# Kernel tuning notes

Measured on AMD Instinct MI355X. Metric: run time of the kernel, lower is better.

## Reference

```python
import jax, jax.numpy as jnp
import numpy as np

B, S, D, H = 2, 2048, 1024, 16
DK = D // H
THETA = 10000.0


def _freqs_cos_sin(dim, seq_len, theta=THETA):
    # matches precompute_freqs_cis: freqs over full d_model, pairs of adjacent dims
    inv = 1.0 / theta ** (np.arange(0, dim, 2)[: dim // 2].astype(np.float32) / dim)
    t = np.arange(seq_len, dtype=np.float32)
    ang = np.outer(t, inv)  # [S, D/2]
    return jnp.asarray(np.cos(ang)), jnp.asarray(np.sin(ang))


def setup_inputs() -> dict:
    key = jax.random.key(0)
    ks = jax.random.split(key, 11)
    sc = 1.0 / np.sqrt(D)
    cos, sin = _freqs_cos_sin(D, S)
    return {
        "query": jax.random.normal(ks[0], (B, S, D), jnp.float32),
        "key": jax.random.normal(ks[1], (B, S, D), jnp.float32),
        "value": jax.random.normal(ks[2], (B, S, D), jnp.float32),
        "wq": jax.random.normal(ks[3], (D, D), jnp.float32) * sc,
        "bq": jnp.zeros((D,), jnp.float32),
        "wk": jax.random.normal(ks[4], (D, D), jnp.float32) * sc,
        "bk": jnp.zeros((D,), jnp.float32),
        "wv": jax.random.normal(ks[5], (D, D), jnp.float32) * sc,
        "bv": jnp.zeros((D,), jnp.float32),
        "wo": jax.random.normal(ks[6], (D, D), jnp.float32) * sc,
        "bo": jnp.zeros((D,), jnp.float32),
        "cos": cos,  # [S, D/2]
        "sin": sin,  # [S, D/2]
    }


def _rope(x, cos, sin):
    # x: [B,S,D]; pairs are adjacent elements along D (view_as_complex semantics)
    xr = x.reshape(*x.shape[:-1], -1, 2)  # [B,S,D/2,2]
    x0, x1 = xr[..., 0], xr[..., 1]
    c, s = cos[None], sin[None]  # broadcast over batch
    o0 = x0 * c - x1 * s
    o1 = x0 * s + x1 * c
    return jnp.stack([o0, o1], axis=-1).reshape(x.shape)


def reference(query, key, value, wq, bq, wk, bk, wv, bv, wo, bo, cos, sin):
    q = query @ wq.T + bq
    k = key @ wk.T + bk
    v = value @ wv.T + bv
    q = _rope(q, cos, sin)
    k = _rope(k, cos, sin)
    # split heads: [B,S,D] -> [B,H,S,DK]
    q = q.reshape(B, S, H, DK).transpose(0, 2, 1, 3)
    k = k.reshape(B, S, H, DK).transpose(0, 2, 1, 3)
    v = v.reshape(B, S, H, DK).transpose(0, 2, 1, 3)
    scores = jnp.einsum("bhqd,bhkd->bhqk", q, k) / jnp.sqrt(jnp.float32(DK))
    attn = jax.nn.softmax(scores, axis=-1)  # dropout is identity in eval
    out = jnp.einsum("bhqk,bhkd->bhqd", attn, v)
    out = out.transpose(0, 2, 1, 3).reshape(B, S, D)
    return out @ wo.T + bo
```

## Files before the change

kernel.cpp:

```cpp
#include <hip/hip_runtime.h>
#include <hip/hip_fp16.h>

typedef _Float16 f16;
using f16x8 = __attribute__((ext_vector_type(8))) _Float16;
using h2 = __attribute__((ext_vector_type(2))) __fp16;
using f32x4 = __attribute__((ext_vector_type(4))) float;
using f32x16 = __attribute__((ext_vector_type(16))) float;

#define LOG2E 1.4426950408889634f

__device__ __forceinline__ void gload16(const void* g, void* l) {
  __builtin_amdgcn_global_load_lds(
      (const __attribute__((address_space(1))) void*)g,
      (__attribute__((address_space(3))) void*)l, 16, 0, 0);
}

__device__ __forceinline__ float b32(h2 x) { return __builtin_bit_cast(float, x); }
__device__ __forceinline__ unsigned u32(h2 x) { return __builtin_bit_cast(unsigned, x); }

__global__ __launch_bounds__(256) void convert_k(
    const float* __restrict__ q, const float* __restrict__ k, const float* __restrict__ v,
    const float* __restrict__ wq, const float* __restrict__ wk,
    const float* __restrict__ wv, const float* __restrict__ wo,
    f16* __restrict__ dst) {
  const size_t SEG = (size_t)4 * 1024 * 1024;
  size_t i = ((size_t)blockIdx.x * 256 + threadIdx.x) * 8;
  const float* src; size_t off;
  if (i < SEG)            { src = q;  off = i; }
  else if (i < 2 * SEG)   { src = k;  off = i - SEG; }
  else if (i < 3 * SEG)   { src = v;  off = i - 2 * SEG; }
  else {
    size_t wi = i - 3 * SEG;
    int s = (int)(wi >> 20);
    src = (s == 0) ? wq : (s == 1) ? wk : (s == 2) ? wv : wo;
    off = wi & ((1u << 20) - 1);
  }
  float4 a = *(const float4*)(src + off);
  float4 b = *(const float4*)(src + off + 4);
  f16x8 o;
  o[0] = (f16)a.x; o[1] = (f16)a.y; o[2] = (f16)a.z; o[3] = (f16)a.w;
  o[4] = (f16)b.x; o[5] = (f16)b.y; o[6] = (f16)b.z; o[7] = (f16)b.w;
  *(f16x8*)(dst + i) = o;
}

template <int QKV>
__global__ __launch_bounds__(256) void gemm_k(
    const f16* __restrict__ Abase, const f16* __restrict__ Wbase,
    const float* __restrict__ b0, const float* __restrict__ b1, const float* __restrict__ b2,
    const float* __restrict__ cosT, const float* __restrict__ sinT,
    f16* __restrict__ qh, f16* __restrict__ kh, f16* __restrict__ vt,
    float* __restrict__ outF) {
  __shared__ f16 sm[6][128 * 32];
  int tid = threadIdx.x, wid = tid >> 6, lane = tid & 63;
  int z = QKV ? blockIdx.z : 0;
  const f16* A = Abase + (size_t)z * (4u * 1024 * 1024);
  const f16* W = Wbase + (size_t)z * (1024u * 1024);

  int lid = blockIdx.x + (blockIdx.y << 3);
  int xcd = lid & 7, q = lid >> 3;
  int m0 = (xcd * 4 + (q & 3)) * 128;
  int n0 = (q >> 2) * 128;
  int wr = wid >> 1, wc = wid & 1;
  f32x4 acc[4][4] = {};

  int srow = tid >> 2;
  int sslot = (tid & 3) ^ (srow & 3);
  const f16* asrc0 = A + (size_t)(m0 + srow) * 1024 + sslot * 8;
  const f16* asrc1 = A + (size_t)(m0 + 64 + srow) * 1024 + sslot * 8;
  const f16* bsrc0 = W + (size_t)(n0 + srow) * 1024 + sslot * 8;
  const f16* bsrc1 = W + (size_t)(n0 + 64 + srow) * 1024 + sslot * 8;

  int aoff[4], boff[4];
#pragma unroll
  for (int i = 0; i < 4; ++i) {
    int row = wr * 64 + i * 16 + (lane & 15);
    aoff[i] = row * 32 + (((lane >> 4) ^ (row & 3)) * 8);
    int col = wc * 64 + i * 16 + (lane & 15);
    boff[i] = col * 32 + (((lane >> 4) ^ (col & 3)) * 8);
  }

#define GSTAGE(KT, BUF)                                                        \
  do {                                                                         \
    int k0_ = (KT) * 32;                                                       \
    gload16(asrc0 + k0_, (void*)(&sm[BUF][0] + wid * 512));                    \
    gload16(asrc1 + k0_, (void*)(&sm[BUF][0] + 2048 + wid * 512));             \
    gload16(bsrc0 + k0_, (void*)(&sm[3 + (BUF)][0] + wid * 512));              \
    gload16(bsrc1 + k0_, (void*)(&sm[3 + (BUF)][0] + 2048 + wid * 512));       \
  } while (0)

  GSTAGE(0, 0);
  GSTAGE(1, 1);

  for (int kt = 0; kt < 32; ++kt) {
    int cb = kt % 3;
    if (kt + 2 < 32) {
      GSTAGE(kt + 2, (kt + 2) % 3);
      asm volatile("s_waitcnt vmcnt(8)" ::: "memory");
    } else if (kt + 1 < 32) {
      asm volatile("s_waitcnt vmcnt(4)" ::: "memory");
    } else {
      asm volatile("s_waitcnt vmcnt(0)" ::: "memory");
    }
    __builtin_amdgcn_s_barrier();
    __builtin_amdgcn_sched_barrier(0);
    f16x8 af[4], bf[4];
#pragma unroll
    for (int i = 0; i < 4; ++i) {
      af[i] = *(const f16x8*)(&sm[cb][0] + aoff[i]);
      bf[i] = *(const f16x8*)(&sm[3 + cb][0] + boff[i]);
    }
#pragma unroll
    for (int i = 0; i < 4; ++i)
#pragma unroll
      for (int j = 0; j < 4; ++j)
        acc[i][j] = __builtin_amdgcn_mfma_f32_16x16x32_f16(af[i], bf[j], acc[i][j], 0, 0, 0);
    __builtin_amdgcn_s_barrier();
  }
#undef GSTAGE

  const float* bias = QKV ? (z == 0 ? b0 : (z == 1 ? b1 : b2)) : b0;

  if (QKV) {
    f16* Ct = &sm[0][0];
#pragma unroll
    for (int i = 0; i < 4; ++i) {
#pragma unroll
      for (int j = 0; j < 4; ++j) {
#pragma unroll
        for (int r = 0; r < 4; ++r) {
          int row_l = wr * 64 + i * 16 + ((lane >> 4) << 2) + r;
          int col_l = wc * 64 + j * 16 + (lane & 15);
          int gcol = n0 + col_l;
          float val = acc[i][j][r] + bias[gcol];
          if (z < 2) {
            int s = (m0 + row_l) & 2047;
            float pr = __shfl_xor(val, 1);
            int j2 = gcol >> 1;
            float c = cosT[s * 512 + j2], sn = sinT[s * 512 + j2];
            val = (lane & 1) ? (c * val + sn * pr) : (c * val - sn * pr);
            if (z == 0) val *= 0.125f * LOG2E;
          }
          Ct[row_l * 128 + (col_l ^ ((row_l & 7) << 3))] = (f16)val;
        }
      }
    }
    __syncthreads();
    int bb = m0 >> 11, sbase = m0 & 2047;
    if (z < 2) {
      int row = tid >> 1, halfsel = tid & 1;
      int h = (n0 >> 6) + halfsel;
      f16* dst = (z == 0 ? qh : kh) +
                 (((size_t)bb * 16 + h) * 2048 + sbase + row) * 64;
#pragma unroll
      for (int ch = 0; ch < 8; ++ch) {
        int c = halfsel * 64 + ch * 8;
        f16x8 v = *(const f16x8*)(Ct + row * 128 + (c ^ ((row & 7) << 3)));
        *(f16x8*)(dst + ch * 8) = v;
      }
    } else {
      int c = tid & 127, halfsel = tid >> 7;
      int h = (n0 >> 6) + (c >> 6), dk = c & 63;
      f16* dst = vt + (((size_t)bb * 16 + h) * 64 + dk) * 2048 + sbase + halfsel * 64;
#pragma unroll
      for (int g = 0; g < 8; ++g) {
        f16x8 v;
#pragma unroll
        for (int e = 0; e < 8; ++e) {
          int r = halfsel * 64 + g * 8 + e;
          v[e] = Ct[r * 128 + (c ^ ((r & 7) << 3))];
        }
        *(f16x8*)(dst + g * 8) = v;
      }
    }
  } else {
#pragma unroll
    for (int i = 0; i < 4; ++i) {
#pragma unroll
      for (int j = 0; j < 4; ++j) {
#pragma unroll
        for (int r = 0; r < 4; ++r) {
          int grow = m0 + wr * 64 + i * 16 + ((lane >> 4) << 2) + r;
          int gcol = n0 + wc * 64 + j * 16 + (lane & 15);
          outF[(size_t)grow * 1024 + gcol] = acc[i][j][r] + bias[gcol];
        }
      }
    }
  }
}

__global__ __launch_bounds__(512, 4) void flash_k(
    const f16* __restrict__ qh, const f16* __restrict__ kh, const f16* __restrict__ vt,
    f16* __restrict__ op, float2* __restrict__ mlbuf) {
  __shared__ f16 Ks[2][64 * 64];
  __shared__ f16 Vs[2][64 * 64];
  int tid = threadIdx.x, wid = tid >> 6, lane = tid & 63;
  int l31 = lane & 31, hi = lane >> 5;
  int bid = blockIdx.x;
  int xcd = bid & 7, t = bid >> 3;
  int qt = t & 7, phi = t >> 3;
  int p = phi * 8 + xcd;
  int h = p & 15, z = p >> 4;
  int b = z >> 1, ks = z & 1;
  size_t bh = (size_t)b * 16 + h;
  const f16* qp = qh + bh * (2048 * 64);
  const f16* kp = kh + bh * (2048 * 64) + (size_t)ks * 1024 * 64;
  const f16* vp = vt + bh * (64 * 2048) + ks * 1024;
  int qrow = qt * 256 + wid * 32 + l31;

  f16x8 qf[4];
#pragma unroll
  for (int kk = 0; kk < 4; ++kk)
    qf[kk] = *(const f16x8*)(qp + (size_t)qrow * 64 + kk * 16 + hi * 8);

  int srow = tid >> 3;
  int sch = (tid & 7) ^ (srow & 7);
  const f16* ksrc = kp + (size_t)srow * 64 + sch * 8;
  const f16* vsrc = vp + (size_t)srow * 2048 + sch * 8;

  int offr[2][4];
#pragma unroll
  for (int kb = 0; kb < 2; ++kb)
#pragma unroll
    for (int kk = 0; kk < 4; ++kk) {
      int row = kb * 32 + l31;
      offr[kb][kk] = (row * 128 + kk * 32 + hi * 16) ^ ((row & 7) << 4);
    }

  float m_ = -1e30f, l_ = 0.f;
  f32x16 oacc[2] = {};

  gload16(ksrc, (char*)&Ks[0][0] + tid * 16);
  gload16(vsrc, (char*)&Vs[0][0] + tid * 16);

  int cur = 0;
  for (int kt = 0; kt < 16; ++kt) {
    if (kt < 15) {
      gload16(ksrc + (size_t)(kt + 1) * 4096, (char*)&Ks[cur ^ 1][0] + tid * 16);
      gload16(vsrc + (size_t)(kt + 1) * 64, (char*)&Vs[cur ^ 1][0] + tid * 16);
      asm volatile("s_waitcnt vmcnt(2)" ::: "memory");
    } else {
      asm volatile("s_waitcnt vmcnt(0)" ::: "memory");
    }
    __builtin_amdgcn_s_barrier();
    __builtin_amdgcn_sched_barrier(0);

    const char* kbase = (const char*)&Ks[cur][0];
    f32x16 sacc[2] = {};
    __builtin_amdgcn_s_setprio(1);
#pragma unroll
    for (int kb = 0; kb < 2; ++kb)
#pragma unroll
      for (int kk = 0; kk < 4; ++kk) {
        f16x8 af = *(const f16x8*)(kbase + offr[kb][kk]);
        sacc[kb] = __builtin_amdgcn_mfma_f32_32x32x16_f16(af, qf[kk], sacc[kb], 0, 0, 0);
      }
    __builtin_amdgcn_s_setprio(0);

    float t16[16];
#pragma unroll
    for (int i = 0; i < 16; ++i) t16[i] = fmaxf(sacc[0][i], sacc[1][i]);
#pragma unroll
    for (int s = 8; s; s >>= 1)
#pragma unroll
      for (int i = 0; i < s; ++i) t16[i] = fmaxf(t16[i], t16[i + s]);
    float pmax = fmaxf(t16[0], __shfl_xor(t16[0], 32));

    if (!__all(pmax <= m_ + 8.0f)) {
      float mn = fmaxf(m_, pmax);
      float al = __builtin_amdgcn_exp2f(m_ - mn);
      m_ = mn;
      l_ *= al;
#pragma unroll
      for (int mb = 0; mb < 2; ++mb)
#pragma unroll
        for (int i = 0; i < 16; ++i) oacc[mb][i] *= al;
    }

#pragma unroll
    for (int kb = 0; kb < 2; ++kb)
#pragma unroll
      for (int i = 0; i < 16; ++i)
        sacc[kb][i] = __builtin_amdgcn_exp2f(sacc[kb][i] - m_);
#pragma unroll
    for (int i = 0; i < 16; ++i) t16[i] = sacc[0][i] + sacc[1][i];
#pragma unroll
    for (int s = 8; s; s >>= 1)
#pragma unroll
      for (int i = 0; i < s; ++i) t16[i] += t16[i + s];
    l_ += t16[0] + __shfl_xor(t16[0], 32);

    f16x8 pa[4];
#pragma unroll
    for (int kk = 0; kk < 4; ++kk) {
      int kb = kk >> 1, c8 = (kk & 1) * 8;
      float wA = b32(__builtin_amdgcn_cvt_pkrtz(sacc[kb][c8 + 0], sacc[kb][c8 + 1]));
      float wB = b32(__builtin_amdgcn_cvt_pkrtz(sacc[kb][c8 + 2], sacc[kb][c8 + 3]));
      float wC = b32(__builtin_amdgcn_cvt_pkrtz(sacc[kb][c8 + 4], sacc[kb][c8 + 5]));
      float wD = b32(__builtin_amdgcn_cvt_pkrtz(sacc[kb][c8 + 6], sacc[kb][c8 + 7]));
      float uAC = hi ? wA : wC;
      float uBD = hi ? wB : wD;
      float sAC = __shfl_xor(uAC, 32);
      float sBD = __shfl_xor(uBD, 32);
      float4 ff;
      ff.x = hi ? sAC : wA;
      ff.y = hi ? sBD : wB;
      ff.z = hi ? wC : sAC;
      ff.w = hi ? wD : sBD;
      pa[kk] = __builtin_bit_cast(f16x8, ff);
    }

    const char* vbase = (const char*)&Vs[cur][0];
    __builtin_amdgcn_s_setprio(1);
#pragma unroll
    for (int kk = 0; kk < 4; ++kk)
#pragma unroll
      for (int mb = 0; mb < 2; ++mb) {
        f16x8 av = *(const f16x8*)(vbase + offr[mb][kk]);
        oacc[mb] = __builtin_amdgcn_mfma_f32_32x32x16_f16(av, pa[kk], oacc[mb], 0, 0, 0);
      }
    __builtin_amdgcn_s_setprio(0);

    __builtin_amdgcn_s_barrier();
    cur ^= 1;
  }

  float inv = 1.f / l_;
  f16* orow = op + (((size_t)z * 16 + h) * 2048 + qrow) * 64;
#pragma unroll
  for (int mb = 0; mb < 2; ++mb)
#pragma unroll
    for (int g = 0; g < 4; ++g) {
      uint2 st;
      st.x = u32(__builtin_amdgcn_cvt_pkrtz(oacc[mb][4 * g + 0] * inv, oacc[mb][4 * g + 1] * inv));
      st.y = u32(__builtin_amdgcn_cvt_pkrtz(oacc[mb][4 * g + 2] * inv, oacc[mb][4 * g + 3] * inv));
      *(uint2*)(orow + mb * 32 + g * 8 + hi * 4) = st;
    }
  if (hi == 0)
    mlbuf[((size_t)z * 16 + h) * 2048 + qrow] = make_float2(m_, l_);
}

__global__ __launch_bounds__(256) void combine_k(
    const f16* __restrict__ op, const float2* __restrict__ ml, f16* __restrict__ attnout) {
  int t = blockIdx.x * 256 + threadIdx.x;
  int row = t >> 3, c8 = t & 7;
  int b = row >> 15, h = (row >> 11) & 15, qrow = row & 2047;
  size_t i0 = ((size_t)(b * 2 + 0) * 16 + h) * 2048 + qrow;
  size_t i1 = ((size_t)(b * 2 + 1) * 16 + h) * 2048 + qrow;
  float2 a = ml[i0], c = ml[i1];
  float M = fmaxf(a.x, c.x);
  float w1 = a.y * __builtin_amdgcn_exp2f(a.x - M);
  float w2 = c.y * __builtin_amdgcn_exp2f(c.x - M);
  float inv = 1.f / (w1 + w2);
  w1 *= inv; w2 *= inv;
  f16x8 o1 = *(const f16x8*)(op + i0 * 64 + c8 * 8);
  f16x8 o2 = *(const f16x8*)(op + i1 * 64 + c8 * 8);
  f16x8 o;
#pragma unroll
  for (int e = 0; e < 8; ++e)
    o[e] = (f16)(w1 * (float)o1[e] + w2 * (float)o2[e]);
  *(f16x8*)(attnout + ((size_t)b * 2048 + qrow) * 1024 + h * 64 + c8 * 8) = o;
}

extern "C" void kernel_launch(void* const* d_in, const int* in_sizes, int n_in,
                              void* d_out, int out_size, void* d_ws, size_t ws_size,
                              hipStream_t stream) {
  (void)in_sizes; (void)n_in; (void)out_size; (void)ws_size;
  const float* query = (const float*)d_in[0];
  const float* key   = (const float*)d_in[1];
  const float* value = (const float*)d_in[2];
  const float* wq = (const float*)d_in[3];
  const float* bq = (const float*)d_in[4];
  const float* wk = (const float*)d_in[5];
  const float* bk = (const float*)d_in[6];
  const float* wv = (const float*)d_in[7];
  const float* bv = (const float*)d_in[8];
  const float* wo = (const float*)d_in[9];
  const float* bo = (const float*)d_in[10];
  const float* cosT = (const float*)d_in[11];
  const float* sinT = (const float*)d_in[12];
  float* out = (float*)d_out;
  f16* ws = (f16*)d_ws;
  const size_t SEG = (size_t)4 * 1024 * 1024;
  f16* Xh = ws;
  f16* Wh = ws + 3 * SEG;
  f16* qh = ws + 16u * 1024 * 1024;
  f16* kh = qh + SEG;
  f16* vt = kh + SEG;
  f16* attnout = ws;
  f16* op = ws + SEG;
  float2* mlb = (float2*)(ws + 12u * 1024 * 1024);

  convert_k<<<8192, 256, 0, stream>>>(query, key, value, wq, wk, wv, wo, ws);
  gemm_k<1><<<dim3(8, 32, 3), 256, 0, stream>>>(Xh, Wh, bq, bk, bv, cosT, sinT,
                                                qh, kh, vt, nullptr);
  flash_k<<<512, 512, 0, stream>>>(qh, kh, vt, op, mlb);
  combine_k<<<2048, 256, 0, stream>>>(op, mlb, attnout);
  gemm_k<0><<<dim3(8, 32, 1), 256, 0, stream>>>(attnout, Wh + 3u * 1024 * 1024, bo,
                                                nullptr, nullptr, nullptr, nullptr,
                                                nullptr, nullptr, nullptr, out);
}
```

Before: 141.8 us.

## Triple-buffer flash K/V loads and drop trailing per-iteration barriers

Result: no change. 144.0 us (+1.6%).

```diff
diff --git a/kernel.cpp b/kernel.cpp
--- a/kernel.cpp
+++ b/kernel.cpp
@@ -93,16 +93,14 @@
 
   for (int kt = 0; kt < 32; ++kt) {
     int cb = kt % 3;
-    if (kt + 2 < 32) {
-      GSTAGE(kt + 2, (kt + 2) % 3);
-      asm volatile("s_waitcnt vmcnt(8)" ::: "memory");
-    } else if (kt + 1 < 32) {
+    if (kt < 31) {
       asm volatile("s_waitcnt vmcnt(4)" ::: "memory");
     } else {
       asm volatile("s_waitcnt vmcnt(0)" ::: "memory");
     }
     __builtin_amdgcn_s_barrier();
     __builtin_amdgcn_sched_barrier(0);
+    if (kt + 2 < 32) GSTAGE(kt + 2, (kt + 2) % 3);
     f16x8 af[4], bf[4];
 #pragma unroll
     for (int i = 0; i < 4; ++i) {
@@ -114,9 +112,9 @@
 #pragma unroll
       for (int j = 0; j < 4; ++j)
         acc[i][j] = __builtin_amdgcn_mfma_f32_16x16x32_f16(af[i], bf[j], acc[i][j], 0, 0, 0);
-    __builtin_amdgcn_s_barrier();
   }
 #undef GSTAGE
+  __syncthreads();
 
   const float* bias = QKV ? (z == 0 ? b0 : (z == 1 ? b1 : b2)) : b0;
 
@@ -191,8 +189,8 @@
 __global__ __launch_bounds__(512, 4) void flash_k(
     const f16* __restrict__ qh, const f16* __restrict__ kh, const f16* __restrict__ vt,
     f16* __restrict__ op, float2* __restrict__ mlbuf) {
-  __shared__ f16 Ks[2][64 * 64];
-  __shared__ f16 Vs[2][64 * 64];
+  __shared__ f16 Ks[3][64 * 64];
+  __shared__ f16 Vs[3][64 * 64];
   int tid = threadIdx.x, wid = tid >> 6, lane = tid & 63;
   int l31 = lane & 31, hi = lane >> 5;
   int bid = blockIdx.x;
@@ -231,20 +229,24 @@
 
   gload16(ksrc, (char*)&Ks[0][0] + tid * 16);
   gload16(vsrc, (char*)&Vs[0][0] + tid * 16);
-
-  int cur = 0;
+  gload16(ksrc + 4096, (char*)&Ks[1][0] + tid * 16);
+  gload16(vsrc + 64, (char*)&Vs[1][0] + tid * 16);
+
   for (int kt = 0; kt < 16; ++kt) {
+    int cb = kt % 3;
     if (kt < 15) {
-      gload16(ksrc + (size_t)(kt + 1) * 4096, (char*)&Ks[cur ^ 1][0] + tid * 16);
-      gload16(vsrc + (size_t)(kt + 1) * 64, (char*)&Vs[cur ^ 1][0] + tid * 16);
       asm volatile("s_waitcnt vmcnt(2)" ::: "memory");
     } else {
       asm volatile("s_waitcnt vmcnt(0)" ::: "memory");
     }
     __builtin_amdgcn_s_barrier();
     __builtin_amdgcn_sched_barrier(0);
-
-    const char* kbase = (const char*)&Ks[cur][0];
+    if (kt + 2 < 16) {
+      gload16(ksrc + (size_t)(kt + 2) * 4096, (char*)&Ks[(kt + 2) % 3][0] + tid * 16);
+      gload16(vsrc + (size_t)(kt + 2) * 64, (char*)&Vs[(kt + 2) % 3][0] + tid * 16);
+    }
+
+    const char* kbase = (const char*)&Ks[cb][0];
     f32x16 sacc[2] = {};
     __builtin_amdgcn_s_setprio(1);
 #pragma unroll
@@ -259,11 +261,13 @@
     float t16[16];
 #pragma unroll
     for (int i = 0; i < 16; ++i) t16[i] = fmaxf(sacc[0][i], sacc[1][i]);
-#pragma unroll
-    for (int s = 8; s; s >>= 1)
-#pragma unroll
-      for (int i = 0; i < s; ++i) t16[i] = fmaxf(t16[i], t16[i + s]);
-    float pmax = fmaxf(t16[0], __shfl_xor(t16[0], 32));
+    float v0 = fmaxf(fmaxf(t16[0], t16[1]), t16[2]);
+    float v1 = fmaxf(fmaxf(t16[3], t16[4]), t16[5]);
+    float v2 = fmaxf(fmaxf(t16[6], t16[7]), t16[8]);
+    float v3 = fmaxf(fmaxf(t16[9], t16[10]), t16[11]);
+    float v4 = fmaxf(fmaxf(t16[12], t16[13]), t16[14]);
+    float pl = fmaxf(fmaxf(fmaxf(v0, v1), v2), fmaxf(fmaxf(v3, v4), t16[15]));
+    float pmax = fmaxf(pl, __shfl_xor(pl, 32));
 
     if (!__all(pmax <= m_ + 8.0f)) {
       float mn = fmaxf(m_, pmax);
@@ -309,7 +313,7 @@
       pa[kk] = __builtin_bit_cast(f16x8, ff);
     }
 
-    const char* vbase = (const char*)&Vs[cur][0];
+    const char* vbase = (const char*)&Vs[cb][0];
     __builtin_amdgcn_s_setprio(1);
 #pragma unroll
     for (int kk = 0; kk < 4; ++kk)
@@ -319,9 +323,6 @@
         oacc[mb] = __builtin_amdgcn_mfma_f32_32x32x16_f16(av, pa[kk], oacc[mb], 0, 0, 0);
       }
     __builtin_amdgcn_s_setprio(0);
-
-    __builtin_amdgcn_s_barrier();
-    cur ^= 1;
   }
 
   float inv = 1.f / l_;
```

## Triple-buffer K/V and software-pipeline QK^T one tile ahead in flash kernel

Applied to the files above, without the earlier changes.

Measured after the change: 146.2 us. 3.1% more time.

```diff
diff --git a/kernel.cpp b/kernel.cpp
--- a/kernel.cpp
+++ b/kernel.cpp
@@ -188,11 +188,11 @@
   }
 }
 
-__global__ __launch_bounds__(512, 4) void flash_k(
+__global__ __launch_bounds__(512) void flash_k(
     const f16* __restrict__ qh, const f16* __restrict__ kh, const f16* __restrict__ vt,
     f16* __restrict__ op, float2* __restrict__ mlbuf) {
-  __shared__ f16 Ks[2][64 * 64];
-  __shared__ f16 Vs[2][64 * 64];
+  __shared__ f16 Ks[3][64 * 64];
+  __shared__ f16 Vs[3][64 * 64];
   int tid = threadIdx.x, wid = tid >> 6, lane = tid & 63;
   int l31 = lane & 31, hi = lane >> 5;
   int bid = blockIdx.x;
@@ -231,30 +231,50 @@
 
   gload16(ksrc, (char*)&Ks[0][0] + tid * 16);
   gload16(vsrc, (char*)&Vs[0][0] + tid * 16);
-
-  int cur = 0;
-  for (int kt = 0; kt < 16; ++kt) {
-    if (kt < 15) {
-      gload16(ksrc + (size_t)(kt + 1) * 4096, (char*)&Ks[cur ^ 1][0] + tid * 16);
-      gload16(vsrc + (size_t)(kt + 1) * 64, (char*)&Vs[cur ^ 1][0] + tid * 16);
-      asm volatile("s_waitcnt vmcnt(2)" ::: "memory");
-    } else {
-      asm volatile("s_waitcnt vmcnt(0)" ::: "memory");
-    }
-    __builtin_amdgcn_s_barrier();
-    __builtin_amdgcn_sched_barrier(0);
-
-    const char* kbase = (const char*)&Ks[cur][0];
-    f32x16 sacc[2] = {};
+  gload16(ksrc + 4096, (char*)&Ks[1][0] + tid * 16);
+  gload16(vsrc + 64, (char*)&Vs[1][0] + tid * 16);
+  asm volatile("s_waitcnt vmcnt(0)" ::: "memory");
+  __builtin_amdgcn_s_barrier();
+  __builtin_amdgcn_sched_barrier(0);
+
+  f32x16 sacc2[2][2];
+  {
+    const char* kbase = (const char*)&Ks[0][0];
+    sacc2[0][0] = f32x16{}; sacc2[0][1] = f32x16{};
     __builtin_amdgcn_s_setprio(1);
 #pragma unroll
     for (int kb = 0; kb < 2; ++kb)
 #pragma unroll
       for (int kk = 0; kk < 4; ++kk) {
         f16x8 af = *(const f16x8*)(kbase + offr[kb][kk]);
-        sacc[kb] = __builtin_amdgcn_mfma_f32_32x32x16_f16(af, qf[kk], sacc[kb], 0, 0, 0);
+        sacc2[0][kb] = __builtin_amdgcn_mfma_f32_32x32x16_f16(af, qf[kk], sacc2[0][kb], 0, 0, 0);
       }
     __builtin_amdgcn_s_setprio(0);
+  }
+
+#pragma unroll
+  for (int kt = 0; kt < 16; ++kt) {
+    const int cb = kt % 3, nb = (kt + 1) % 3, pb = (kt + 2) % 3;
+    if (kt + 2 < 16) {
+      gload16(ksrc + (size_t)(kt + 2) * 4096, (char*)&Ks[pb][0] + tid * 16);
+      gload16(vsrc + (size_t)(kt + 2) * 64, (char*)&Vs[pb][0] + tid * 16);
+    }
+    if (kt + 1 < 16) {
+      const char* kbase = (const char*)&Ks[nb][0];
+      sacc2[(kt + 1) & 1][0] = f32x16{}; sacc2[(kt + 1) & 1][1] = f32x16{};
+      __builtin_amdgcn_s_setprio(1);
+#pragma unroll
+      for (int kb = 0; kb < 2; ++kb)
+#pragma unroll
+        for (int kk = 0; kk < 4; ++kk) {
+          f16x8 af = *(const f16x8*)(kbase + offr[kb][kk]);
+          sacc2[(kt + 1) & 1][kb] =
+              __builtin_amdgcn_mfma_f32_32x32x16_f16(af, qf[kk], sacc2[(kt + 1) & 1][kb], 0, 0, 0);
+        }
+      __builtin_amdgcn_s_setprio(0);
+    }
+
+    f32x16* sacc = sacc2[kt & 1];
 
     float t16[16];
 #pragma unroll
@@ -309,7 +329,7 @@
       pa[kk] = __builtin_bit_cast(f16x8, ff);
     }
 
-    const char* vbase = (const char*)&Vs[cur][0];
+    const char* vbase = (const char*)&Vs[cb][0];
     __builtin_amdgcn_s_setprio(1);
 #pragma unroll
     for (int kk = 0; kk < 4; ++kk)
@@ -320,8 +340,9 @@
       }
     __builtin_amdgcn_s_setprio(0);
 
+    asm volatile("s_waitcnt vmcnt(0)" ::: "memory");
     __builtin_amdgcn_s_barrier();
-    cur ^= 1;
+    __builtin_amdgcn_sched_barrier(0);
   }
 
   float inv = 1.f / l_;
```

## Fuse split-KV combine into output projection GEMM prologue

Applied to the files above, without the earlier changes.

Result: slower. 153.1 us (+8.0%).

```diff
diff --git a/kernel.cpp b/kernel.cpp
--- a/kernel.cpp
+++ b/kernel.cpp
@@ -43,16 +43,14 @@
   *(f16x8*)(dst + i) = o;
 }
 
-template <int QKV>
 __global__ __launch_bounds__(256) void gemm_k(
     const f16* __restrict__ Abase, const f16* __restrict__ Wbase,
     const float* __restrict__ b0, const float* __restrict__ b1, const float* __restrict__ b2,
     const float* __restrict__ cosT, const float* __restrict__ sinT,
-    f16* __restrict__ qh, f16* __restrict__ kh, f16* __restrict__ vt,
-    float* __restrict__ outF) {
+    f16* __restrict__ qh, f16* __restrict__ kh, f16* __restrict__ vt) {
   __shared__ f16 sm[6][128 * 32];
   int tid = threadIdx.x, wid = tid >> 6, lane = tid & 63;
-  int z = QKV ? blockIdx.z : 0;
+  int z = blockIdx.z;
   const f16* A = Abase + (size_t)z * (4u * 1024 * 1024);
   const f16* W = Wbase + (size_t)z * (1024u * 1024);
 
@@ -118,71 +116,173 @@
   }
 #undef GSTAGE
 
-  const float* bias = QKV ? (z == 0 ? b0 : (z == 1 ? b1 : b2)) : b0;
-
-  if (QKV) {
-    f16* Ct = &sm[0][0];
-#pragma unroll
-    for (int i = 0; i < 4; ++i) {
-#pragma unroll
-      for (int j = 0; j < 4; ++j) {
-#pragma unroll
-        for (int r = 0; r < 4; ++r) {
-          int row_l = wr * 64 + i * 16 + ((lane >> 4) << 2) + r;
-          int col_l = wc * 64 + j * 16 + (lane & 15);
-          int gcol = n0 + col_l;
-          float val = acc[i][j][r] + bias[gcol];
-          if (z < 2) {
-            int s = (m0 + row_l) & 2047;
-            float pr = __shfl_xor(val, 1);
-            int j2 = gcol >> 1;
-            float c = cosT[s * 512 + j2], sn = sinT[s * 512 + j2];
-            val = (lane & 1) ? (c * val + sn * pr) : (c * val - sn * pr);
-            if (z == 0) val *= 0.125f * LOG2E;
-          }
-          Ct[row_l * 128 + (col_l ^ ((row_l & 7) << 3))] = (f16)val;
+  const float* bias = (z == 0) ? b0 : (z == 1 ? b1 : b2);
+
+  f16* Ct = &sm[0][0];
+#pragma unroll
+  for (int i = 0; i < 4; ++i) {
+#pragma unroll
+    for (int j = 0; j < 4; ++j) {
+#pragma unroll
+      for (int r = 0; r < 4; ++r) {
+        int row_l = wr * 64 + i * 16 + ((lane >> 4) << 2) + r;
+        int col_l = wc * 64 + j * 16 + (lane & 15);
+        int gcol = n0 + col_l;
+        float val = acc[i][j][r] + bias[gcol];
+        if (z < 2) {
+          int s = (m0 + row_l) & 2047;
+          float pr = __shfl_xor(val, 1);
+          int j2 = gcol >> 1;
+          float c = cosT[s * 512 + j2], sn = sinT[s * 512 + j2];
+          val = (lane & 1) ? (c * val + sn * pr) : (c * val - sn * pr);
+          if (z == 0) val *= 0.125f * LOG2E;
         }
+        Ct[row_l * 128 + (col_l ^ ((row_l & 7) << 3))] = (f16)val;
       }
     }
-    __syncthreads();
-    int bb = m0 >> 11, sbase = m0 & 2047;
-    if (z < 2) {
-      int row = tid >> 1, halfsel = tid & 1;
-      int h = (n0 >> 6) + halfsel;
-      f16* dst = (z == 0 ? qh : kh) +
-                 (((size_t)bb * 16 + h) * 2048 + sbase + row) * 64;
-#pragma unroll
-      for (int ch = 0; ch < 8; ++ch) {
-        int c = halfsel * 64 + ch * 8;
-        f16x8 v = *(const f16x8*)(Ct + row * 128 + (c ^ ((row & 7) << 3)));
-        *(f16x8*)(dst + ch * 8) = v;
+  }
+  __syncthreads();
+  int bb = m0 >> 11, sbase = m0 & 2047;
+  if (z < 2) {
+    int row = tid >> 1, halfsel = tid & 1;
+    int h = (n0 >> 6) + halfsel;
+    f16* dst = (z == 0 ? qh : kh) +
+               (((size_t)bb * 16 + h) * 2048 + sbase + row) * 64;
+#pragma unroll
+    for (int ch = 0; ch < 8; ++ch) {
+      int c = halfsel * 64 + ch * 8;
+      f16x8 v = *(const f16x8*)(Ct + row * 128 + (c ^ ((row & 7) << 3)));
+      *(f16x8*)(dst + ch * 8) = v;
+    }
+  } else {
+    int c = tid & 127, halfsel = tid >> 7;
+    int h = (n0 >> 6) + (c >> 6), dk = c & 63;
+    f16* dst = vt + (((size_t)bb * 16 + h) * 64 + dk) * 2048 + sbase + halfsel * 64;
+#pragma unroll
+    for (int g = 0; g < 8; ++g) {
+      f16x8 v;
+#pragma unroll
+      for (int e = 0; e < 8; ++e) {
+        int r = halfsel * 64 + g * 8 + e;
+        v[e] = Ct[r * 128 + (c ^ ((r & 7) << 3))];
       }
-    } else {
-      int c = tid & 127, halfsel = tid >> 7;
-      int h = (n0 >> 6) + (c >> 6), dk = c & 63;
-      f16* dst = vt + (((size_t)bb * 16 + h) * 64 + dk) * 2048 + sbase + halfsel * 64;
-#pragma unroll
-      for (int g = 0; g < 8; ++g) {
-        f16x8 v;
-#pragma unroll
-        for (int e = 0; e < 8; ++e) {
-          int r = halfsel * 64 + g * 8 + e;
-          v[e] = Ct[r * 128 + (c ^ ((r & 7) << 3))];
-        }
-        *(f16x8*)(dst + g * 8) = v;
-      }
-    }
-  } else {
-#pragma unroll
-    for (int i = 0; i < 4; ++i) {
-#pragma unroll
-      for (int j = 0; j < 4; ++j) {
-#pragma unroll
-        for (int r = 0; r < 4; ++r) {
-          int grow = m0 + wr * 64 + i * 16 + ((lane >> 4) << 2) + r;
-          int gcol = n0 + wc * 64 + j * 16 + (lane & 15);
-          outF[(size_t)grow * 1024 + gcol] = acc[i][j][r] + bias[gcol];
-        }
+      *(f16x8*)(dst + g * 8) = v;
+    }
+  }
+}
+
+__global__ __launch_bounds__(256) void oproj_k(
+    const f16* __restrict__ op, const float2* __restrict__ ml,
+    const f16* __restrict__ W, const float* __restrict__ bo,
+    float* __restrict__ outF) {
+  __shared__ f16 sm[3 * 4096 + 3 * 2048];
+#define SMA(B) (sm + (B) * 4096)
+#define SMB(B) (sm + 12288 + (B) * 2048)
+  int tid = threadIdx.x, wid = tid >> 6, lane = tid & 63;
+
+  int lid = blockIdx.x + blockIdx.y * gridDim.x;
+  int xcd = lid & 7, q = lid >> 3;
+  int m0 = (xcd * 4 + (q & 3)) * 128;
+  int n0 = (q >> 2) * 64;
+  int wr = wid >> 1, wc = wid & 1;
+  f32x4 acc[4][2] = {};
+
+  int srow = tid >> 2;
+  int sslot = (tid & 3) ^ (srow & 3);
+  int bA = m0 >> 11;
+  int q0 = (m0 & 2047) + srow;
+  int q1 = q0 + 64;
+  const f16* bsrc = W + (size_t)(n0 + srow) * 1024 + sslot * 8;
+
+  int aoff[4], boff[2];
+#pragma unroll
+  for (int i = 0; i < 4; ++i) {
+    int row = wr * 64 + i * 16 + (lane & 15);
+    aoff[i] = row * 32 + (((lane >> 4) ^ (row & 3)) * 8);
+  }
+#pragma unroll
+  for (int j = 0; j < 2; ++j) {
+    int col = wc * 32 + j * 16 + (lane & 15);
+    boff[j] = col * 32 + (((lane >> 4) ^ (col & 3)) * 8);
+  }
+
+  f16x8 rO1[2][2], rO2[2][2], rB[2];
+  float2 rM1[2][2], rM2[2][2];
+
+#define LOADG(KT, S)                                                            \
+  do {                                                                          \
+    int c_ = (KT) * 32 + sslot * 8;                                             \
+    int hh_ = c_ >> 6, dk_ = c_ & 63;                                           \
+    size_t i0a = (((size_t)(bA * 2 + 0) * 16 + hh_) * 2048 + q0);               \
+    size_t i1a = (((size_t)(bA * 2 + 1) * 16 + hh_) * 2048 + q0);               \
+    size_t i0b = (((size_t)(bA * 2 + 0) * 16 + hh_) * 2048 + q1);               \
+    size_t i1b = (((size_t)(bA * 2 + 1) * 16 + hh_) * 2048 + q1);               \
+    rO1[S][0] = *(const f16x8*)(op + i0a * 64 + dk_);                           \
+    rO2[S][0] = *(const f16x8*)(op + i1a * 64 + dk_);                           \
+    rO1[S][1] = *(const f16x8*)(op + i0b * 64 + dk_);                           \
+    rO2[S][1] = *(const f16x8*)(op + i1b * 64 + dk_);                           \
+    rM1[S][0] = ml[i0a]; rM2[S][0] = ml[i1a];                                   \
+    rM1[S][1] = ml[i0b]; rM2[S][1] = ml[i1b];                                   \
+    rB[S] = *(const f16x8*)(bsrc + (KT) * 32);                                  \
+  } while (0)
+
+#define CWRITE(BUF, S)                                                          \
+  do {                                                                          \
+    _Pragma("unroll")                                                           \
+    for (int p_ = 0; p_ < 2; ++p_) {                                            \
+      float2 a_ = rM1[S][p_], c_ = rM2[S][p_];                                  \
+      float M_ = fmaxf(a_.x, c_.x);                                             \
+      float w1_ = a_.y * __builtin_amdgcn_exp2f(a_.x - M_);                     \
+      float w2_ = c_.y * __builtin_amdgcn_exp2f(c_.x - M_);                     \
+      float inv_ = 1.f / (w1_ + w2_);                                           \
+      w1_ *= inv_; w2_ *= inv_;                                                 \
+      f16x8 o_;                                                                 \
+      _Pragma("unroll")                                                         \
+      for (int e_ = 0; e_ < 8; ++e_)                                            \
+        o_[e_] = (f16)(w1_ * (float)rO1[S][p_][e_] + w2_ * (float)rO2[S][p_][e_]); \
+      *(f16x8*)(SMA(BUF) + p_ * 2048 + tid * 8) = o_;                           \
+    }                                                                           \
+    *(f16x8*)(SMB(BUF) + tid * 8) = rB[S];                                      \
+  } while (0)
+
+  LOADG(0, 0);
+  LOADG(1, 1);
+  CWRITE(0, 0);
+
+#pragma unroll
+  for (int kt = 0; kt < 32; ++kt) {
+    const int cb = kt % 3;
+    if (kt + 2 < 32) LOADG(kt + 2, kt & 1);
+    if (kt + 1 < 32) CWRITE((kt + 1) % 3, (kt + 1) & 1);
+    asm volatile("s_waitcnt lgkmcnt(0)" ::: "memory");
+    __builtin_amdgcn_s_barrier();
+    __builtin_amdgcn_sched_barrier(0);
+    f16x8 af[4], bf[2];
+#pragma unroll
+    for (int i = 0; i < 4; ++i) af[i] = *(const f16x8*)(SMA(cb) + aoff[i]);
+#pragma unroll
+    for (int j = 0; j < 2; ++j) bf[j] = *(const f16x8*)(SMB(cb) + boff[j]);
+#pragma unroll
+    for (int i = 0; i < 4; ++i)
+#pragma unroll
+      for (int j = 0; j < 2; ++j)
+        acc[i][j] = __builtin_amdgcn_mfma_f32_16x16x32_f16(af[i], bf[j], acc[i][j], 0, 0, 0);
+    __builtin_amdgcn_s_barrier();
+  }
+#undef LOADG
+#undef CWRITE
+#undef SMA
+#undef SMB
+
+#pragma unroll
+  for (int i = 0; i < 4; ++i) {
+#pragma unroll
+    for (int j = 0; j < 2; ++j) {
+#pragma unroll
+      for (int r = 0; r < 4; ++r) {
+        int grow = m0 + wr * 64 + i * 16 + ((lane >> 4) << 2) + r;
+        int gcol = n0 + wc * 32 + j * 16 + (lane & 15);
+        outF[(size_t)grow * 1024 + gcol] = acc[i][j][r] + bo[gcol];
       }
     }
   }
@@ -337,28 +437,6 @@
     }
   if (hi == 0)
     mlbuf[((size_t)z * 16 + h) * 2048 + qrow] = make_float2(m_, l_);
-}
-
-__global__ __launch_bounds__(256) void combine_k(
-    const f16* __restrict__ op, const float2* __restrict__ ml, f16* __restrict__ attnout) {
-  int t = blockIdx.x * 256 + threadIdx.x;
-  int row = t >> 3, c8 = t & 7;
-  int b = row >> 15, h = (row >> 11) & 15, qrow = row & 2047;
-  size_t i0 = ((size_t)(b * 2 + 0) * 16 + h) * 2048 + qrow;
-  size_t i1 = ((size_t)(b * 2 + 1) * 16 + h) * 2048 + qrow;
-  float2 a = ml[i0], c = ml[i1];
-  float M = fmaxf(a.x, c.x);
-  float w1 = a.y * __builtin_amdgcn_exp2f(a.x - M);
-  float w2 = c.y * __builtin_amdgcn_exp2f(c.x - M);
-  float inv = 1.f / (w1 + w2);
-  w1 *= inv; w2 *= inv;
-  f16x8 o1 = *(const f16x8*)(op + i0 * 64 + c8 * 8);
-  f16x8 o2 = *(const f16x8*)(op + i1 * 64 + c8 * 8);
-  f16x8 o;
-#pragma unroll
-  for (int e = 0; e < 8; ++e)
-    o[e] = (f16)(w1 * (float)o1[e] + w2 * (float)o2[e]);
-  *(f16x8*)(attnout + ((size_t)b * 2048 + qrow) * 1024 + h * 64 + c8 * 8) = o;
 }
 
 extern "C" void kernel_launch(void* const* d_in, const int* in_sizes, int n_in,
@@ -386,16 +464,12 @@
   f16* qh = ws + 16u * 1024 * 1024;
   f16* kh = qh + SEG;
   f16* vt = kh + SEG;
-  f16* attnout = ws;
   f16* op = ws + SEG;
   float2* mlb = (float2*)(ws + 12u * 1024 * 1024);
 
   convert_k<<<8192, 256, 0, stream>>>(query, key, value, wq, wk, wv, wo, ws);
-  gemm_k<1><<<dim3(8, 32, 3), 256, 0, stream>>>(Xh, Wh, bq, bk, bv, cosT, sinT,
-                                                qh, kh, vt, nullptr);
+  gemm_k<<<dim3(8, 32, 3), 256, 0, stream>>>(Xh, Wh, bq, bk, bv, cosT, sinT,
+                                             qh, kh, vt);
   flash_k<<<512, 512, 0, stream>>>(qh, kh, vt, op, mlb);
-  combine_k<<<2048, 256, 0, stream>>>(op, mlb, attnout);
-  gemm_k<0><<<dim3(8, 32, 1), 256, 0, stream>>>(attnout, Wh + 3u * 1024 * 1024, bo,
-                                                nullptr, nullptr, nullptr, nullptr,
-                                                nullptr, nullptr, nullptr, out);
-}
+  oproj_k<<<dim3(16, 32), 256, 0, stream>>>(op, mlb, Wh + 3u * 1024 * 1024, bo, out);
+}
```
